# Performance work log

Hardware: AMD Instinct MI355X
Metric: run time of the kernel (lower is better)

## Reference

```python
import jax, jax.numpy as jnp
import numpy as np

N = 50000   # nodes per graph
D = 256     # embedding dim
E = 800000  # edges per graph
NEG_SLOPE = 0.2
EPS = 1e-9


def gat_layer(h, src, dst, W, a):
    # SpGraphAttentionLayer: transform, edge attention exp(-leakyrelu(a.[h_i||h_j])),
    # softmax-normalized scatter aggregation, ELU activation.
    h = h @ W                                   # [N, D]
    # a.[h_src || h_dst] == (h @ a[:D])[src] + (h @ a[D:])[dst]  (avoids [E,2D] concat)
    alpha_src = h @ a[:D]                       # [N]
    alpha_dst = h @ a[D:]                       # [N]
    logits = alpha_src[src] + alpha_dst[dst]    # [E]
    e = jnp.exp(-jax.nn.leaky_relu(logits, NEG_SLOPE))  # [E], pyGAT sparse form
    rowsum = jax.ops.segment_sum(e, src, num_segments=N)            # [N]
    num = jax.ops.segment_sum(e[:, None] * h[dst], src, num_segments=N)  # [N, D]
    out = num / (rowsum[:, None] + EPS)
    return jax.nn.elu(out)


def setup_inputs() -> dict:
    key = jax.random.key(0)
    ks = jax.random.split(key, 8)
    w_std = float(np.sqrt(2.0 / (D + D)))  # xavier
    sr_emb = jax.random.normal(ks[0], (N, D), jnp.float32) * w_std
    tg_emb = jax.random.normal(ks[1], (N, D), jnp.float32) * w_std
    W1 = jax.random.normal(ks[2], (D, D), jnp.float32) * w_std
    a1 = jax.random.normal(ks[3], (2 * D,), jnp.float32) * 0.1
    W2 = jax.random.normal(ks[4], (D, D), jnp.float32) * w_std
    a2 = jax.random.normal(ks[5], (2 * D,), jnp.float32) * 0.1
    adj_sr = jax.random.randint(ks[6], (2, E), 0, N, dtype=jnp.int64)
    adj_tg = jax.random.randint(ks[7], (2, E), 0, N, dtype=jnp.int64)
    return {"sr_emb": sr_emb, "tg_emb": tg_emb, "W1": W1, "a1": a1,
            "W2": W2, "a2": a2, "adj_sr": adj_sr, "adj_tg": adj_tg}


def reference(sr_emb, tg_emb, W1, a1, W2, a2, adj_sr, adj_tg):
    # layers are shared across the two graphs (same ModuleList applied to both)
    src_s, dst_s = adj_sr[0], adj_sr[1]
    src_t, dst_t = adj_tg[0], adj_tg[1]
    for (W, a) in ((W1, a1), (W2, a2)):
        sr_emb = gat_layer(sr_emb, src_s, dst_s, W, a)
        tg_emb = gat_layer(tg_emb, src_t, dst_t, W, a)
    return (sr_emb, tg_emb)
```

## Files before the change

### kernel.cpp

```cpp
#include <hip/hip_runtime.h>

#define NEG_SLOPE 0.2f
#define EPS_ 1e-9f

typedef __attribute__((ext_vector_type(8))) short short8v;
typedef __attribute__((ext_vector_type(4))) float f32x4;

__device__ __forceinline__ float bf2f(unsigned short u) {
    return __uint_as_float(((unsigned)u) << 16);
}
__device__ __forceinline__ unsigned short f2bf(float f) {
    unsigned u = __float_as_uint(f);
    u = u + 0x7FFFu + ((u >> 16) & 1u);
    return (unsigned short)(u >> 16);
}

__global__ void hist_kernel(const int* __restrict__ src, int* __restrict__ cnt, int E) {
    int i = blockIdx.x * blockDim.x + threadIdx.x;
    if (i < E) atomicAdd(&cnt[src[i]], 1);
}

__global__ __launch_bounds__(256) void scan1_kernel(const int* __restrict__ cnt,
        int* __restrict__ locpre, int* __restrict__ blocksum, int n) {
    int t = threadIdx.x;
    int lane = t & 63, wid = t >> 6;
    int base = blockIdx.x * 1024 + t * 4;
    int4 v = {0, 0, 0, 0};
    if (base + 3 < n) {
        v = *(const int4*)(cnt + base);
    } else {
        if (base + 0 < n) v.x = cnt[base + 0];
        if (base + 1 < n) v.y = cnt[base + 1];
        if (base + 2 < n) v.z = cnt[base + 2];
        if (base + 3 < n) v.w = cnt[base + 3];
    }
    int s = v.x + v.y + v.z + v.w;
    int incl = s;
    for (int off = 1; off < 64; off <<= 1) {
        int u = __shfl_up(incl, off);
        if (lane >= off) incl += u;
    }
    __shared__ int ws[4];
    if (lane == 63) ws[wid] = incl;
    __syncthreads();
    int woff = 0;
    for (int i = 0; i < wid; ++i) woff += ws[i];
    int excl = incl - s + woff;
    int4 o;
    o.x = excl; o.y = excl + v.x; o.z = o.y + v.y; o.w = o.z + v.z;
    if (base + 3 < n) {
        *(int4*)(locpre + base) = o;
    } else {
        if (base + 0 < n) locpre[base + 0] = o.x;
        if (base + 1 < n) locpre[base + 1] = o.y;
        if (base + 2 < n) locpre[base + 2] = o.z;
        if (base + 3 < n) locpre[base + 3] = o.w;
    }
    if (t == 255) blocksum[blockIdx.x] = excl + s;
}

__global__ __launch_bounds__(64) void scan2_kernel(int* __restrict__ blocksum, int nb) {
    int lane = threadIdx.x;
    int carry = 0;
    for (int base = 0; base < nb; base += 64) {
        int v = (base + lane < nb) ? blocksum[base + lane] : 0;
        int incl = v;
        for (int off = 1; off < 64; off <<= 1) {
            int u = __shfl_up(incl, off);
            if (lane >= off) incl += u;
        }
        int tot = __shfl(incl, 63);
        if (base + lane < nb) blocksum[base + lane] = incl - v + carry;
        carry += tot;
    }
}

__global__ __launch_bounds__(256) void scan3_kernel(const int* __restrict__ locpre,
        const int* __restrict__ blocksum, int* __restrict__ row_ptr,
        int* __restrict__ cursor, int n, int total) {
    int base = blockIdx.x * 1024 + threadIdx.x * 4;
    int off = blocksum[blockIdx.x];
    if (base + 3 < n) {
        int4 v = *(const int4*)(locpre + base);
        v.x += off; v.y += off; v.z += off; v.w += off;
        *(int4*)(row_ptr + base) = v;
        *(int4*)(cursor + base) = v;
    } else {
        for (int i = 0; i < 4; ++i) {
            if (base + i < n) {
                int v = locpre[base + i] + off;
                row_ptr[base + i] = v;
                cursor[base + i] = v;
            }
        }
    }
    if (blockIdx.x == 0 && threadIdx.x == 0) row_ptr[n] = total;
}

__global__ void scatter_kernel(const int* __restrict__ src, const int* __restrict__ dst,
        int* __restrict__ cursor, int* __restrict__ colv, int E) {
    int i = blockIdx.x * blockDim.x + threadIdx.x;
    if (i < E) {
        int p = atomicAdd(&cursor[src[i]], 1);
        colv[p] = dst[i];
    }
}

__global__ void wt_kernel(const float* __restrict__ W, short* __restrict__ Wt) {
    int nn = blockIdx.x, k = threadIdx.x;
    Wt[nn * 256 + k] = (short)f2bf(W[k * 256 + nn]);
}

template<bool IN_BF16>
__global__ __launch_bounds__(256) void gemm_kernel(const void* __restrict__ hin,
        const short* __restrict__ Wt, short* __restrict__ hp, int M) {
    __shared__ short As[64 * 40];
    __shared__ short Bt[256 * 40];
    int tid = threadIdx.x;
    int lane = tid & 63, w = tid >> 6;
    int m0 = blockIdx.x * 64;

    f32x4 acc[16];
#pragma unroll
    for (int t = 0; t < 16; ++t) acc[t] = (f32x4){0.f, 0.f, 0.f, 0.f};

    int ar = tid >> 2;
    int ac = (tid & 3) * 8;
    int agrow = m0 + ar;

    for (int kk = 0; kk < 256; kk += 32) {
        short8v av = (short8v){0,0,0,0,0,0,0,0};
        if constexpr (IN_BF16) {
            if (agrow < M)
                av = *(const short8v*)((const short*)hin + (size_t)agrow * 256 + kk + ac);
        } else {
            if (agrow < M) {
                const float* s = (const float*)hin + (size_t)agrow * 256 + kk + ac;
                float4 v0 = *(const float4*)s;
                float4 v1 = *(const float4*)(s + 4);
                av[0] = (short)f2bf(v0.x); av[1] = (short)f2bf(v0.y);
                av[2] = (short)f2bf(v0.z); av[3] = (short)f2bf(v0.w);
                av[4] = (short)f2bf(v1.x); av[5] = (short)f2bf(v1.y);
                av[6] = (short)f2bf(v1.z); av[7] = (short)f2bf(v1.w);
            }
        }
        *(short8v*)&As[ar * 40 + ac] = av;
        {
            const short* s = Wt + (size_t)tid * 256 + kk;
#pragma unroll
            for (int i = 0; i < 4; ++i)
                *(short8v*)&Bt[tid * 40 + i * 8] = *(const short8v*)(s + i * 8);
        }
        __syncthreads();
        short8v a = *(const short8v*)&As[(16 * w + (lane & 15)) * 40 + (lane >> 4) * 8];
#pragma unroll
        for (int t = 0; t < 16; ++t) {
            short8v b = *(const short8v*)&Bt[(16 * t + (lane & 15)) * 40 + (lane >> 4) * 8];
            acc[t] = __builtin_amdgcn_mfma_f32_16x16x32_bf16(a, b, acc[t], 0, 0, 0);
        }
        __syncthreads();
    }
    int r0 = 16 * w + (lane >> 4) * 4;
    int c0 = lane & 15;
#pragma unroll
    for (int t = 0; t < 16; ++t) {
#pragma unroll
        for (int j = 0; j < 4; ++j) {
            int grow = m0 + r0 + j;
            if (grow < M) hp[(size_t)grow * 256 + 16 * t + c0] = (short)f2bf(acc[t][j]);
        }
    }
}

__global__ __launch_bounds__(256) void alpha_kernel(const unsigned short* __restrict__ hp,
        const float* __restrict__ a, float* __restrict__ asrc, float* __restrict__ adst, int M) {
    int gw = (blockIdx.x * blockDim.x + threadIdx.x) >> 6;
    int lane = threadIdx.x & 63;
    if (gw >= M) return;
    ushort4 hv = *(const ushort4*)(hp + (size_t)gw * 256 + lane * 4);
    float h0 = bf2f(hv.x), h1 = bf2f(hv.y), h2 = bf2f(hv.z), h3 = bf2f(hv.w);
    float4 a0 = *(const float4*)(a + lane * 4);
    float4 a1 = *(const float4*)(a + 256 + lane * 4);
    float s0 = h0 * a0.x + h1 * a0.y + h2 * a0.z + h3 * a0.w;
    float s1 = h0 * a1.x + h1 * a1.y + h2 * a1.z + h3 * a1.w;
    for (int off = 32; off > 0; off >>= 1) {
        s0 += __shfl_xor(s0, off);
        s1 += __shfl_xor(s1, off);
    }
    if (lane == 0) { asrc[gw] = s0; adst[gw] = s1; }
}

template<bool OUT_BF16>
__global__ __launch_bounds__(256) void aggregate_kernel(const int* __restrict__ row_ptr,
        const int* __restrict__ colv, const float* __restrict__ asrc,
        const float* __restrict__ adst, const unsigned short* __restrict__ hp,
        void* __restrict__ outp, int n) {
    int node = (blockIdx.x * blockDim.x + threadIdx.x) >> 6;
    int lane = threadIdx.x & 63;
    if (node >= n) return;
    int beg = row_ptr[node], end = row_ptr[node + 1];
    float ai = asrc[node];
    float acc0 = 0.f, acc1 = 0.f, acc2 = 0.f, acc3 = 0.f, rs = 0.f;
    for (int cur = beg; cur < end; cur += 64) {
        int cnt = min(64, end - cur);
        int j = 0;
        float wgt = 0.f;
        if (lane < cnt) {
            j = colv[cur + lane];
            float x = ai + adst[j];
            float lr = x > 0.f ? x : NEG_SLOPE * x;
            wgt = __expf(-lr);
        }
        for (int k = 0; k < cnt; ++k) {
            int jk = __shfl(j, k);
            float wk = __shfl(wgt, k);
            ushort4 hv = *(const ushort4*)(hp + (size_t)jk * 256 + lane * 4);
            acc0 += wk * bf2f(hv.x);
            acc1 += wk * bf2f(hv.y);
            acc2 += wk * bf2f(hv.z);
            acc3 += wk * bf2f(hv.w);
            rs += wk;
        }
    }
    float inv = 1.f / (rs + EPS_);
    float v0 = acc0 * inv, v1 = acc1 * inv, v2 = acc2 * inv, v3 = acc3 * inv;
    v0 = v0 > 0.f ? v0 : __expf(v0) - 1.f;
    v1 = v1 > 0.f ? v1 : __expf(v1) - 1.f;
    v2 = v2 > 0.f ? v2 : __expf(v2) - 1.f;
    v3 = v3 > 0.f ? v3 : __expf(v3) - 1.f;
    if constexpr (OUT_BF16) {
        ushort4 o;
        o.x = f2bf(v0); o.y = f2bf(v1); o.z = f2bf(v2); o.w = f2bf(v3);
        *(ushort4*)((unsigned short*)outp + (size_t)node * 256 + lane * 4) = o;
    } else {
        float4 o = {v0, v1, v2, v3};
        *(float4*)((float*)outp + (size_t)node * 256 + lane * 4) = o;
    }
}

extern "C" void kernel_launch(void* const* d_in, const int* in_sizes, int n_in,
                              void* d_out, int out_size, void* d_ws, size_t ws_size,
                              hipStream_t stream) {
    const float* sr_emb = (const float*)d_in[0];
    const float* tg_emb = (const float*)d_in[1];
    const float* W1 = (const float*)d_in[2];
    const float* a1 = (const float*)d_in[3];
    const float* W2 = (const float*)d_in[4];
    const float* a2 = (const float*)d_in[5];
    const int* adj_sr = (const int*)d_in[6];
    const int* adj_tg = (const int*)d_in[7];
    int N = in_sizes[0] / 256;
    int E = in_sizes[6] / 2;

    char* p = (char*)d_ws;
    auto alloc = [&](size_t bytes) -> void* {
        void* r = (void*)p;
        p += (bytes + 255) & ~(size_t)255;
        return r;
    };
    int nb = (N + 1023) / 1024;
    int* cnt      = (int*)alloc((size_t)N * 4);
    int* row_ptr  = (int*)alloc((size_t)(N + 1) * 4);
    int* cursor   = (int*)alloc((size_t)N * 4);
    int* locpre   = (int*)alloc((size_t)N * 4);
    int* blocksum = (int*)alloc((size_t)nb * 4);
    int* colv     = (int*)alloc((size_t)E * 4);
    short* Wt1    = (short*)alloc(256 * 256 * 2);
    short* Wt2    = (short*)alloc(256 * 256 * 2);
    short* hp     = (short*)alloc((size_t)N * 256 * 2);
    float* asrc   = (float*)alloc((size_t)N * 4);
    float* adst   = (float*)alloc((size_t)N * 4);
    short* tmp    = (short*)alloc((size_t)N * 256 * 2);

    wt_kernel<<<256, 256, 0, stream>>>(W1, Wt1);
    wt_kernel<<<256, 256, 0, stream>>>(W2, Wt2);

    int gemm_grid = (N + 63) / 64;
    int nw_grid = (N + 3) / 4;
    int e_grid = (E + 255) / 256;

    for (int g = 0; g < 2; ++g) {
        const int* srcv = (g == 0 ? adj_sr : adj_tg);
        const int* dstv = srcv + E;
        const float* emb = (g == 0 ? sr_emb : tg_emb);
        float* outg = (float*)d_out + (size_t)g * N * 256;

        hipMemsetAsync(cnt, 0, (size_t)N * 4, stream);
        hist_kernel<<<e_grid, 256, 0, stream>>>(srcv, cnt, E);
        scan1_kernel<<<nb, 256, 0, stream>>>(cnt, locpre, blocksum, N);
        scan2_kernel<<<1, 64, 0, stream>>>(blocksum, nb);
        scan3_kernel<<<nb, 256, 0, stream>>>(locpre, blocksum, row_ptr, cursor, N, E);
        scatter_kernel<<<e_grid, 256, 0, stream>>>(srcv, dstv, cursor, colv, E);

        gemm_kernel<false><<<gemm_grid, 256, 0, stream>>>(emb, Wt1, hp, N);
        alpha_kernel<<<nw_grid, 256, 0, stream>>>((const unsigned short*)hp, a1, asrc, adst, N);
        aggregate_kernel<true><<<nw_grid, 256, 0, stream>>>(row_ptr, colv, asrc, adst,
                (const unsigned short*)hp, tmp, N);
        gemm_kernel<true><<<gemm_grid, 256, 0, stream>>>(tmp, Wt2, hp, N);
        alpha_kernel<<<nw_grid, 256, 0, stream>>>((const unsigned short*)hp, a2, asrc, adst, N);
        aggregate_kernel<false><<<nw_grid, 256, 0, stream>>>(row_ptr, colv, asrc, adst,
                (const unsigned short*)hp, outg, N);
    }
}
```

Measured before the change: 606.6 us.

## Fuse alpha projection into GEMM epilogue and batch neighbor gathers in aggregation

The attention projections alpha_src and alpha_dst are now computed in the GEMM epilogue from fp32 accumulators, with a 16-lane shuffle reduction, so the separate alpha kernel and its re-read of hp are gone. The aggregation loop now loads 16 neighbor indices, their adst values and their feature rows up front before accumulating. This exposes more memory-level parallelism than the earlier serial shuffle-per-edge loop. The trade-offs are more registers in both kernels, and alpha is now computed from unrounded fp32 values instead of bf16.

```diff
diff --git a/kernel.cpp b/kernel.cpp
--- a/kernel.cpp
+++ b/kernel.cpp
@@ -113,7 +113,9 @@
 
 template<bool IN_BF16>
 __global__ __launch_bounds__(256) void gemm_kernel(const void* __restrict__ hin,
-        const short* __restrict__ Wt, short* __restrict__ hp, int M) {
+        const short* __restrict__ Wt, short* __restrict__ hp,
+        const float* __restrict__ af, float* __restrict__ asrc,
+        float* __restrict__ adst, int M) {
     __shared__ short As[64 * 40];
     __shared__ short Bt[256 * 40];
     int tid = threadIdx.x;
@@ -162,32 +164,29 @@
     }
     int r0 = 16 * w + (lane >> 4) * 4;
     int c0 = lane & 15;
+    float a_s[16], a_d[16];
 #pragma unroll
     for (int t = 0; t < 16; ++t) {
-#pragma unroll
-        for (int j = 0; j < 4; ++j) {
-            int grow = m0 + r0 + j;
-            if (grow < M) hp[(size_t)grow * 256 + 16 * t + c0] = (short)f2bf(acc[t][j]);
-        }
-    }
-}
-
-__global__ __launch_bounds__(256) void alpha_kernel(const unsigned short* __restrict__ hp,
-        const float* __restrict__ a, float* __restrict__ asrc, float* __restrict__ adst, int M) {
-    int gw = (blockIdx.x * blockDim.x + threadIdx.x) >> 6;
-    int lane = threadIdx.x & 63;
-    if (gw >= M) return;
-    ushort4 hv = *(const ushort4*)(hp + (size_t)gw * 256 + lane * 4);
-    float h0 = bf2f(hv.x), h1 = bf2f(hv.y), h2 = bf2f(hv.z), h3 = bf2f(hv.w);
-    float4 a0 = *(const float4*)(a + lane * 4);
-    float4 a1 = *(const float4*)(a + 256 + lane * 4);
-    float s0 = h0 * a0.x + h1 * a0.y + h2 * a0.z + h3 * a0.w;
-    float s1 = h0 * a1.x + h1 * a1.y + h2 * a1.z + h3 * a1.w;
-    for (int off = 32; off > 0; off >>= 1) {
-        s0 += __shfl_xor(s0, off);
-        s1 += __shfl_xor(s1, off);
-    }
-    if (lane == 0) { asrc[gw] = s0; adst[gw] = s1; }
+        a_s[t] = af[16 * t + c0];
+        a_d[t] = af[256 + 16 * t + c0];
+    }
+#pragma unroll
+    for (int j = 0; j < 4; ++j) {
+        int grow = m0 + r0 + j;
+        float ssrc = 0.f, sdst = 0.f;
+#pragma unroll
+        for (int t = 0; t < 16; ++t) {
+            float cv = acc[t][j];
+            ssrc = fmaf(cv, a_s[t], ssrc);
+            sdst = fmaf(cv, a_d[t], sdst);
+            if (grow < M) hp[(size_t)grow * 256 + 16 * t + c0] = (short)f2bf(cv);
+        }
+        for (int off = 1; off < 16; off <<= 1) {
+            ssrc += __shfl_xor(ssrc, off);
+            sdst += __shfl_xor(sdst, off);
+        }
+        if (c0 == 0 && grow < M) { asrc[grow] = ssrc; adst[grow] = sdst; }
+    }
 }
 
 template<bool OUT_BF16>
@@ -198,29 +197,33 @@
     int node = (blockIdx.x * blockDim.x + threadIdx.x) >> 6;
     int lane = threadIdx.x & 63;
     if (node >= n) return;
+    node = __builtin_amdgcn_readfirstlane(node);
     int beg = row_ptr[node], end = row_ptr[node + 1];
     float ai = asrc[node];
+    const ushort4* __restrict__ hpv = (const ushort4*)hp;
     float acc0 = 0.f, acc1 = 0.f, acc2 = 0.f, acc3 = 0.f, rs = 0.f;
-    for (int cur = beg; cur < end; cur += 64) {
-        int cnt = min(64, end - cur);
-        int j = 0;
-        float wgt = 0.f;
-        if (lane < cnt) {
-            j = colv[cur + lane];
-            float x = ai + adst[j];
-            float lr = x > 0.f ? x : NEG_SLOPE * x;
-            wgt = __expf(-lr);
-        }
-        for (int k = 0; k < cnt; ++k) {
-            int jk = __shfl(j, k);
-            float wk = __shfl(wgt, k);
-            ushort4 hv = *(const ushort4*)(hp + (size_t)jk * 256 + lane * 4);
-            acc0 += wk * bf2f(hv.x);
-            acc1 += wk * bf2f(hv.y);
-            acc2 += wk * bf2f(hv.z);
-            acc3 += wk * bf2f(hv.w);
-            rs += wk;
-        }
+    for (int e = beg; e < end; e += 16) {
+        int m = end - e;
+        int js[16]; float ds[16]; ushort4 qs[16];
+#pragma unroll
+        for (int k = 0; k < 16; ++k)
+            if (k < m) { js[k] = colv[e + k]; ds[k] = adst[js[k]]; }
+#pragma unroll
+        for (int k = 0; k < 16; ++k)
+            if (k < m) qs[k] = hpv[(size_t)js[k] * 64 + lane];
+#pragma unroll
+        for (int k = 0; k < 16; ++k)
+            if (k < m) {
+                float x = ai + ds[k];
+                float lr = fmaxf(x, NEG_SLOPE * x);
+                float wk = __expf(-lr);
+                ushort4 q = qs[k];
+                acc0 = fmaf(wk, bf2f(q.x), acc0);
+                acc1 = fmaf(wk, bf2f(q.y), acc1);
+                acc2 = fmaf(wk, bf2f(q.z), acc2);
+                acc3 = fmaf(wk, bf2f(q.w), acc3);
+                rs += wk;
+            }
     }
     float inv = 1.f / (rs + EPS_);
     float v0 = acc0 * inv, v1 = acc1 * inv, v2 = acc2 * inv, v3 = acc3 * inv;
@@ -292,12 +295,10 @@
         scan3_kernel<<<nb, 256, 0, stream>>>(locpre, blocksum, row_ptr, cursor, N, E);
         scatter_kernel<<<e_grid, 256, 0, stream>>>(srcv, dstv, cursor, colv, E);
 
-        gemm_kernel<false><<<gemm_grid, 256, 0, stream>>>(emb, Wt1, hp, N);
-        alpha_kernel<<<nw_grid, 256, 0, stream>>>((const unsigned short*)hp, a1, asrc, adst, N);
+        gemm_kernel<false><<<gemm_grid, 256, 0, stream>>>(emb, Wt1, hp, a1, asrc, adst, N);
         aggregate_kernel<true><<<nw_grid, 256, 0, stream>>>(row_ptr, colv, asrc, adst,
                 (const unsigned short*)hp, tmp, N);
-        gemm_kernel<true><<<gemm_grid, 256, 0, stream>>>(tmp, Wt2, hp, N);
-        alpha_kernel<<<nw_grid, 256, 0, stream>>>((const unsigned short*)hp, a2, asrc, adst, N);
+        gemm_kernel<true><<<gemm_grid, 256, 0, stream>>>(tmp, Wt2, hp, a2, asrc, adst, N);
         aggregate_kernel<false><<<nw_grid, 256, 0, stream>>>(row_ptr, colv, asrc, adst,
                 (const unsigned short*)hp, outg, N);
     }
```

Result: slower. 716.4 us (+18.1%).
